# Kernel tuning notes

Hardware: AMD Instinct MI355X
Metric: run time of the kernel (lower is better)

## Reference

```python
import jax, jax.numpy as jnp
import numpy as np

GROUP_SIZE = 64  # int4 precision
QMAX = 7.0       # symmetric int4 quant scale divisor


def setup_inputs() -> dict:
    key = jax.random.key(0)
    ks = jax.random.split(key, 8)
    B, S, C_in, C_out, R = 1, 4096, 3072, 3072, 32
    G = C_in // GROUP_SIZE
    x = jax.random.normal(ks[0], (B, S, C_in), dtype=jnp.float32)
    # unpacked int4 weight codes in [0,16); reference subtracts 8 -> signed int4 [-8,7]
    qweight = jax.random.randint(ks[1], (C_out, C_in), 0, 16, dtype=jnp.int32)
    # small positive per-group, per-out-channel weight scales
    wscales = jax.random.uniform(ks[2], (G, C_out), dtype=jnp.float32) * 0.01 + 0.001
    # positive smoothing factors bounded away from zero
    smooth_factor = jax.random.uniform(ks[3], (C_in,), dtype=jnp.float32) + 0.5
    proj_down = jax.random.normal(ks[4], (C_in, R), dtype=jnp.float32) * (1.0 / np.sqrt(C_in))
    proj_up = jax.random.normal(ks[5], (C_out, R), dtype=jnp.float32) * (1.0 / np.sqrt(R))
    bias = jax.random.normal(ks[6], (C_out,), dtype=jnp.float32) * 0.02
    return {
        "x": x,
        "qweight": qweight,
        "wscales": wscales,
        "smooth_factor": smooth_factor,
        "proj_down": proj_down,
        "proj_up": proj_up,
        "bias": bias,
    }


def reference(x, qweight, wscales, smooth_factor, proj_down, proj_up, bias):
    B, S, C = x.shape
    C_out = qweight.shape[0]
    M = B * S
    G = C // GROUP_SIZE

    # --- smoothing: x_hat = x / s (SVDQuant smoothing on activations) ---
    xs = x.reshape(M, C) / smooth_factor  # (M, C)

    # --- low-rank branch hidden state (fused with quantization in CUDA kernel) ---
    lora_act = jnp.einsum('mc,cr->mr', xs, proj_down)  # (M, R)

    # --- dynamic per-token, per-group int4 activation quantization ---
    xg = xs.reshape(M, G, GROUP_SIZE)
    amax = jnp.max(jnp.abs(xg), axis=-1, keepdims=True)          # (M, G, 1)
    ascale = amax / QMAX
    q = jnp.clip(jnp.round(xg / jnp.maximum(ascale, 1e-8)), -8.0, 7.0)
    x_dq = (q * ascale).reshape(M, C)                            # dequantized activations

    # --- weight dequantization: signed int4 codes * per-group/out-channel scales ---
    qw = qweight.astype(jnp.float32) - 8.0                       # (C_out, C) in [-8, 7]
    w_dq = (qw.reshape(C_out, G, GROUP_SIZE) * wscales.T[:, :, None]).reshape(C_out, C)

    # --- quantized GEMM + low-rank correction + bias ---
    out = jnp.einsum('mc,oc->mo', x_dq, w_dq)
    out = out + jnp.einsum('mr,or->mo', lora_act, proj_up) + bias
    return out.reshape(B, S, C_out)
```

## Files before the change

kernel.cpp:

```cpp
#include <hip/hip_runtime.h>
#include <stdint.h>

typedef unsigned short u16;

#define MTOK 4096
#define CIN  3072
#define COUT 3072
#define RANK 32
#define KT48 48
#define RS   3136
#define LKSPLIT 16
#define LKC (CIN/LKSPLIT)


typedef __attribute__((ext_vector_type(8))) short bf16x8;
typedef __attribute__((ext_vector_type(4))) float f32x4;

__device__ __forceinline__ u16 f2bf(float f) {
  union { float f; unsigned u; } v; v.f = f;
  unsigned r = v.u + 0x7FFFu + ((v.u >> 16) & 1u);
  return (u16)(r >> 16);
}

__device__ __forceinline__ void gload_lds16(const void* g, void* l) {
  __builtin_amdgcn_global_load_lds(
      (const __attribute__((address_space(1))) unsigned int*)g,
      (__attribute__((address_space(3))) unsigned int*)l, 16, 0, 0);
}

__device__ __forceinline__ float quant1(float xs, float ascale, float qd) {
  float q = rintf(xs / qd);
  q = fminf(fmaxf(q, -8.f), 7.f);
  return q * ascale;
}


__global__ __launch_bounds__(256) void wdq_kernel(
    const int* __restrict__ qw, const float* __restrict__ wsc,
    const float* __restrict__ pu, u16* __restrict__ wdq, u16* __restrict__ pu_bf)
{
  const int o = blockIdx.x;
  const int t = threadIdx.x;
  const int4* qrow = (const int4*)(qw + (size_t)o * CIN);
  u16* orow = wdq + (size_t)o * RS;
#pragma unroll
  for (int p = 0; p < 3; ++p) {
    const int c4 = p * 256 + t;
    const int g = (c4 * 4) >> 6;
    const float ws = wsc[g * COUT + o];
    const int4 qv = qrow[c4];
    ushort4 ov;
    ov.x = f2bf((float)(qv.x - 8) * ws);
    ov.y = f2bf((float)(qv.y - 8) * ws);
    ov.z = f2bf((float)(qv.z - 8) * ws);
    ov.w = f2bf((float)(qv.w - 8) * ws);
    ((ushort4*)orow)[c4] = ov;
  }
  if (t < RANK) pu_bf[(size_t)o * RANK + t] = f2bf(pu[(size_t)o * RANK + t]);
}

__global__ __launch_bounds__(256) void quant_kernel(
    const float* __restrict__ x, const float* __restrict__ smooth,
    u16* __restrict__ xdq)
{
  const int b = blockIdx.x;
  const int t = threadIdx.x;
  const int m0 = (b >> 4) * 64;
  const int kblk = b & 15;
  const int col = (t & 15) * 4;
#pragma unroll
  for (int kt = 0; kt < 3; ++kt) {
    const int k0 = kblk * LKC + kt * 64;
#pragma unroll
    for (int it = 0; it < 4; ++it) {
      const int row = m0 + it * 16 + (t >> 4);
      const float4 xv = *(const float4*)(x + (size_t)row * CIN + k0 + col);
      const float4 sv = *(const float4*)(smooth + k0 + col);
      const float xs0 = xv.x / sv.x, xs1 = xv.y / sv.y;
      const float xs2 = xv.z / sv.z, xs3 = xv.w / sv.w;
      float a = fmaxf(fmaxf(fabsf(xs0), fabsf(xs1)), fmaxf(fabsf(xs2), fabsf(xs3)));
#pragma unroll
      for (int off = 1; off < 16; off <<= 1) a = fmaxf(a, __shfl_xor(a, off));
      const float ascale = a / 7.0f;
      const float qd = fmaxf(ascale, 1e-8f);
      ushort4 oq;
      oq.x = f2bf(quant1(xs0, ascale, qd));
      oq.y = f2bf(quant1(xs1, ascale, qd));
      oq.z = f2bf(quant1(xs2, ascale, qd));
      oq.w = f2bf(quant1(xs3, ascale, qd));
      *(ushort4*)(xdq + (size_t)row * RS + k0 + col) = oq;
    }
  }
}

__global__ __launch_bounds__(256) void lora_kernel(
    const float* __restrict__ x, const float* __restrict__ smooth,
    const float* __restrict__ pd, float* __restrict__ lp)
{
  __shared__ __align__(16) u16 sA[128 * 64];
  __shared__ __align__(16) u16 sB[32 * 64];
  const int b = blockIdx.x;
  const int t = threadIdx.x;
  const int m0 = (b >> 4) * 128;
  const int kblk = b & 15;
  const int wave = t >> 6, lane = t & 63;
  const int lm = lane & 15, lkq = (lane >> 4) * 8;

  f32x4 acc[2][2];
  const f32x4 fz = {0.f, 0.f, 0.f, 0.f};
#pragma unroll
  for (int i = 0; i < 2; ++i)
#pragma unroll
    for (int j = 0; j < 2; ++j) acc[i][j] = fz;

  for (int kt = 0; kt < LKC / 64; ++kt) {
    const int k0 = kblk * LKC + kt * 64;
    const int col = (t & 15) * 4;
#pragma unroll
    for (int it = 0; it < 8; ++it) {
      const int row = it * 16 + (t >> 4);
      const float4 xv = *(const float4*)(x + (size_t)(m0 + row) * CIN + k0 + col);
      const float4 sv = *(const float4*)(smooth + k0 + col);
      ushort4 ov;
      ov.x = f2bf(xv.x / sv.x); ov.y = f2bf(xv.y / sv.y);
      ov.z = f2bf(xv.z / sv.z); ov.w = f2bf(xv.w / sv.w);
      *(ushort4*)&sA[row * 64 + col] = ov;
    }
#pragma unroll
    for (int i = 0; i < 8; ++i) {
      const int idx = i * 256 + t;
      const int k = idx >> 5, r = idx & 31;
      sB[r * 64 + k] = f2bf(pd[(size_t)(k0 + k) * RANK + r]);
    }
    __syncthreads();
#pragma unroll
    for (int kk = 0; kk < 2; ++kk) {
      const int ko = kk * 32 + lkq;
      bf16x8 af[2], bfr[2];
#pragma unroll
      for (int i = 0; i < 2; ++i)
        af[i] = *(const bf16x8*)&sA[(wave * 32 + i * 16 + lm) * 64 + ko];
#pragma unroll
      for (int j = 0; j < 2; ++j)
        bfr[j] = *(const bf16x8*)&sB[(j * 16 + lm) * 64 + ko];
#pragma unroll
      for (int i = 0; i < 2; ++i)
#pragma unroll
        for (int j = 0; j < 2; ++j)
          acc[i][j] = __builtin_amdgcn_mfma_f32_16x16x32_bf16(af[i], bfr[j], acc[i][j], 0, 0, 0);
    }
    __syncthreads();
  }
  float* lpk = lp + (size_t)kblk * MTOK * RANK;
#pragma unroll
  for (int i = 0; i < 2; ++i)
#pragma unroll
    for (int j = 0; j < 2; ++j) {
      const int col = j * 16 + lm;
      const int row0 = m0 + wave * 32 + i * 16 + (lane >> 4) * 4;
#pragma unroll
      for (int r = 0; r < 4; ++r)
        lpk[(size_t)(row0 + r) * RANK + col] = acc[i][j][r];
    }
}

__global__ __launch_bounds__(256) void lora_fix_kernel(
    const float* __restrict__ lp, u16* __restrict__ lora_bf)
{
  const int idx = blockIdx.x * 256 + threadIdx.x;
  const int m = idx >> 5, c = idx & 31;
  float s = 0.f;
#pragma unroll
  for (int k = 0; k < LKSPLIT; ++k) s += lp[((size_t)k * MTOK + m) * RANK + c];
  lora_bf[(size_t)m * RANK + c] = f2bf(s);
}


__device__ __forceinline__ void stage_half(const u16* __restrict__ g, u16* lds_base,
                                           int kt, int half, int buf, int t) {
#pragma unroll
  for (int r = 0; r < 2; ++r) {
    const int ld = r * 512 + t;
    const int row = ld >> 3;
    const int d = ld & 7;
    const int c16 = d ^ (row & 7);
    gload_lds16(g + (size_t)(half * 128 + row) * RS + kt * 64 + c16 * 8,
                lds_base + buf * 16384 + half * 8192 + ld * 8);
  }
}

#define DSA(buf, mh) \
  _Pragma("unroll") for (int i = 0; i < 4; ++i) { \
    const int rl = wm * 64 + i * 16 + lm; \
    _Pragma("unroll") for (int kk = 0; kk < 2; ++kk) \
      af[i][kk] = *(const bf16x8*)&lds[(buf)*16384 + (mh)*8192 + rl * 64 + \
                    ((((kk << 2) | q4) ^ (rl & 7)) << 3)]; \
  }

#define DSB(buf, nh, BF) \
  _Pragma("unroll") for (int j = 0; j < 2; ++j) { \
    const int rl = wn * 32 + j * 16 + lm; \
    _Pragma("unroll") for (int kk = 0; kk < 2; ++kk) \
      BF[j][kk] = *(const bf16x8*)&lds[32768 + (buf)*16384 + (nh)*8192 + rl * 64 + \
                    ((((kk << 2) | q4) ^ (rl & 7)) << 3)]; \
  }

#define MFMA_Q(mh, nh, BF) \
  __builtin_amdgcn_s_setprio(1); \
  _Pragma("unroll") for (int i = 0; i < 4; ++i) \
  _Pragma("unroll") for (int j = 0; j < 2; ++j) \
  _Pragma("unroll") for (int kk = 0; kk < 2; ++kk) \
    acc[(mh)*4 + i][(nh)*2 + j] = __builtin_amdgcn_mfma_f32_16x16x32_bf16( \
        af[i][kk], BF[j][kk], acc[(mh)*4 + i][(nh)*2 + j], 0, 0, 0); \
  __builtin_amdgcn_s_setprio(0);

#define PH_OPEN() \
  __builtin_amdgcn_sched_barrier(0); \
  __builtin_amdgcn_s_barrier(); \
  asm volatile("s_waitcnt lgkmcnt(0)" ::: "memory"); \
  __builtin_amdgcn_sched_barrier(0)

#define PH_CLOSE() \
  __builtin_amdgcn_sched_barrier(0); \
  __builtin_amdgcn_s_barrier(); \
  __builtin_amdgcn_sched_barrier(0)

#define VM8() asm volatile("s_waitcnt vmcnt(8)" ::: "memory")
#define VM0() asm volatile("s_waitcnt vmcnt(0)" ::: "memory")

#define TILE8(cur, S_A0, S_B0, S_B1, S_A1, VMI) do { \
  DSA(cur, 0); DSB(cur, 0, bf0); \
  PH_OPEN(); MFMA_Q(0, 0, bf0); PH_CLOSE(); \
  DSB(cur, 1, bf1); S_A0; S_B0; \
  PH_OPEN(); MFMA_Q(0, 1, bf1); PH_CLOSE(); \
  DSA(cur, 1); S_B1; \
  PH_OPEN(); MFMA_Q(1, 1, bf1); PH_CLOSE(); \
  S_A1; \
  PH_OPEN(); MFMA_Q(1, 0, bf0); VMI; PH_CLOSE(); \
} while (0)

__global__ __launch_bounds__(512, 2) void gemm_kernel(
    const u16* __restrict__ xdq, const u16* __restrict__ wdq,
    const u16* __restrict__ pu_bf, const u16* __restrict__ lora_bf,
    const float* __restrict__ bias, float* __restrict__ out)
{
  __shared__ __align__(16) u16 lds[65536];

  const int t = threadIdx.x;
  const int wid = t >> 6, lane = t & 63;
  const int wm = wid >> 2, wn = wid & 3;
  const int lm = lane & 15, q4 = lane >> 4;

  const int wg = blockIdx.x;
  const int swz = (wg & 7) * 24 + (wg >> 3);
  const int by = swz / 12, bx = swz % 12;
  const int m0 = by * 256, n0 = bx * 256;

  const u16* Ag = xdq + (size_t)m0 * RS;
  const u16* Bg = wdq + (size_t)n0 * RS;
  u16* ldsB = lds + 32768;

  f32x4 acc[8][4];
  const f32x4 fz = {0.f, 0.f, 0.f, 0.f};
#pragma unroll
  for (int i = 0; i < 8; ++i)
#pragma unroll
    for (int j = 0; j < 4; ++j) acc[i][j] = fz;

  bf16x8 af[4][2], bf0[2][2], bf1[2][2];

  stage_half(Ag, lds,  0, 0, 0, t);
  stage_half(Bg, ldsB, 0, 0, 0, t);
  stage_half(Bg, ldsB, 0, 1, 0, t);
  stage_half(Ag, lds,  0, 1, 0, t);
  stage_half(Ag, lds,  1, 0, 1, t);
  stage_half(Bg, ldsB, 1, 0, 1, t);
  stage_half(Bg, ldsB, 1, 1, 1, t);
  stage_half(Ag, lds,  1, 1, 1, t);
  VM8();
  __builtin_amdgcn_s_barrier();
  __builtin_amdgcn_sched_barrier(0);

  for (int T = 0; T < 46; T += 2) {
    TILE8(0,
          stage_half(Ag, lds,  T + 2, 0, 0, t),
          stage_half(Bg, ldsB, T + 2, 0, 0, t),
          stage_half(Bg, ldsB, T + 2, 1, 0, t),
          stage_half(Ag, lds,  T + 2, 1, 0, t),
          VM8());
    TILE8(1,
          stage_half(Ag, lds,  T + 3, 0, 1, t),
          stage_half(Bg, ldsB, T + 3, 0, 1, t),
          stage_half(Bg, ldsB, T + 3, 1, 1, t),
          stage_half(Ag, lds,  T + 3, 1, 1, t),
          VM8());
  }
  TILE8(0, (void)0, (void)0, (void)0, (void)0, VM0());
  TILE8(1, (void)0, (void)0, (void)0, (void)0, (void)0);

  bf16x8 bl[4];
#pragma unroll
  for (int b = 0; b < 4; ++b) {
    const int bcol = n0 + (b >> 1) * 128 + wn * 32 + (b & 1) * 16 + lm;
    bl[b] = *(const bf16x8*)(pu_bf + (size_t)bcol * RANK + q4 * 8);
  }
#pragma unroll
  for (int a = 0; a < 8; ++a) {
    const int arow = m0 + (a >> 2) * 128 + wm * 64 + (a & 3) * 16 + lm;
    const bf16x8 al = *(const bf16x8*)(lora_bf + (size_t)arow * RANK + q4 * 8);
#pragma unroll
    for (int b = 0; b < 4; ++b)
      acc[a][b] = __builtin_amdgcn_mfma_f32_16x16x32_bf16(al, bl[b], acc[a][b], 0, 0, 0);
  }

#pragma unroll
  for (int b = 0; b < 4; ++b) {
    const int col = n0 + (b >> 1) * 128 + wn * 32 + (b & 1) * 16 + lm;
    const float bv = bias[col];
#pragma unroll
    for (int a = 0; a < 8; ++a) {
      const int row0 = m0 + (a >> 2) * 128 + wm * 64 + (a & 3) * 16 + q4 * 4;
#pragma unroll
      for (int r = 0; r < 4; ++r)
        out[(size_t)(row0 + r) * COUT + col] = acc[a][b][r] + bv;
    }
  }
}

extern "C" void kernel_launch(void* const* d_in, const int* in_sizes, int n_in,
                              void* d_out, int out_size, void* d_ws, size_t ws_size,
                              hipStream_t stream) {
  const float* x      = (const float*)d_in[0];
  const int*   qw     = (const int*)d_in[1];
  const float* wsc    = (const float*)d_in[2];
  const float* smooth = (const float*)d_in[3];
  const float* pd     = (const float*)d_in[4];
  const float* pu     = (const float*)d_in[5];
  const float* bias   = (const float*)d_in[6];
  float* out = (float*)d_out;

  u16* xdq     = (u16*)d_ws;
  u16* wdq     = xdq + (size_t)MTOK * RS;
  u16* pu_bf   = wdq + (size_t)COUT * RS;
  u16* lora_bf = pu_bf + (size_t)COUT * RANK;
  float* lp    = (float*)(lora_bf + (size_t)MTOK * RANK);

  wdq_kernel<<<COUT, 256, 0, stream>>>(qw, wsc, pu, wdq, pu_bf);
  quant_kernel<<<1024, 256, 0, stream>>>(x, smooth, xdq);
  lora_kernel<<<512, 256, 0, stream>>>(x, smooth, pd, lp);
  lora_fix_kernel<<<MTOK * RANK / 256, 256, 0, stream>>>(lp, lora_bf);
  gemm_kernel<<<192, 512, 0, stream>>>(
      xdq, wdq, pu_bf, lora_bf, bias, out);
}
```

Baseline: 251.8 us.

## Fuse weight dequant, activation quant and LoRA down-projection into one prep kernel

```diff
diff --git a/kernel.cpp b/kernel.cpp
--- a/kernel.cpp
+++ b/kernel.cpp
@@ -7,11 +7,10 @@
 #define CIN  3072
 #define COUT 3072
 #define RANK 32
-#define KT48 48
 #define RS   3136
 #define LKSPLIT 16
 #define LKC (CIN/LKSPLIT)
-
+#define WROWS 6
 
 typedef __attribute__((ext_vector_type(8))) short bf16x8;
 typedef __attribute__((ext_vector_type(4))) float f32x4;
@@ -34,50 +33,67 @@
   return q * ascale;
 }
 
-
-__global__ __launch_bounds__(256) void wdq_kernel(
+__global__ __launch_bounds__(256) void prep_kernel(
+    const float* __restrict__ x, const float* __restrict__ smooth,
     const int* __restrict__ qw, const float* __restrict__ wsc,
-    const float* __restrict__ pu, u16* __restrict__ wdq, u16* __restrict__ pu_bf)
-{
-  const int o = blockIdx.x;
-  const int t = threadIdx.x;
-  const int4* qrow = (const int4*)(qw + (size_t)o * CIN);
-  u16* orow = wdq + (size_t)o * RS;
-#pragma unroll
-  for (int p = 0; p < 3; ++p) {
-    const int c4 = p * 256 + t;
-    const int g = (c4 * 4) >> 6;
-    const float ws = wsc[g * COUT + o];
-    const int4 qv = qrow[c4];
-    ushort4 ov;
-    ov.x = f2bf((float)(qv.x - 8) * ws);
-    ov.y = f2bf((float)(qv.y - 8) * ws);
-    ov.z = f2bf((float)(qv.z - 8) * ws);
-    ov.w = f2bf((float)(qv.w - 8) * ws);
-    ((ushort4*)orow)[c4] = ov;
-  }
-  if (t < RANK) pu_bf[(size_t)o * RANK + t] = f2bf(pu[(size_t)o * RANK + t]);
-}
-
-__global__ __launch_bounds__(256) void quant_kernel(
-    const float* __restrict__ x, const float* __restrict__ smooth,
-    u16* __restrict__ xdq)
+    const float* __restrict__ pd, const float* __restrict__ pu,
+    u16* __restrict__ xdq, u16* __restrict__ wdq, u16* __restrict__ pu_bf,
+    float* __restrict__ lp)
 {
   const int b = blockIdx.x;
   const int t = threadIdx.x;
-  const int m0 = (b >> 4) * 64;
+
+#pragma unroll
+  for (int r = 0; r < WROWS; ++r) {
+    const int o = b * WROWS + r;
+    const int4* qrow = (const int4*)(qw + (size_t)o * CIN);
+    u16* orow = wdq + (size_t)o * RS;
+#pragma unroll
+    for (int p = 0; p < 3; ++p) {
+      const int c4 = p * 256 + t;
+      const int g = (c4 * 4) >> 6;
+      const float ws = wsc[g * COUT + o];
+      const int4 qv = qrow[c4];
+      ushort4 ov;
+      ov.x = f2bf((float)(qv.x - 8) * ws);
+      ov.y = f2bf((float)(qv.y - 8) * ws);
+      ov.z = f2bf((float)(qv.z - 8) * ws);
+      ov.w = f2bf((float)(qv.w - 8) * ws);
+      ((ushort4*)orow)[c4] = ov;
+    }
+  }
+  if (t < WROWS * RANK) {
+    const int o = b * WROWS + (t >> 5);
+    pu_bf[(size_t)o * RANK + (t & 31)] = f2bf(pu[(size_t)o * RANK + (t & 31)]);
+  }
+
+  __shared__ __align__(16) u16 sA[128 * 64];
+  __shared__ __align__(16) u16 sB[32 * 64];
+  const int m0 = (b >> 4) * 128;
   const int kblk = b & 15;
-  const int col = (t & 15) * 4;
-#pragma unroll
-  for (int kt = 0; kt < 3; ++kt) {
+  const int wave = t >> 6, lane = t & 63;
+  const int lm = lane & 15, lkq = (lane >> 4) * 8;
+
+  f32x4 acc[2][2];
+  const f32x4 fz = {0.f, 0.f, 0.f, 0.f};
+#pragma unroll
+  for (int i = 0; i < 2; ++i)
+#pragma unroll
+    for (int j = 0; j < 2; ++j) acc[i][j] = fz;
+
+  for (int kt = 0; kt < LKC / 64; ++kt) {
     const int k0 = kblk * LKC + kt * 64;
-#pragma unroll
-    for (int it = 0; it < 4; ++it) {
-      const int row = m0 + it * 16 + (t >> 4);
-      const float4 xv = *(const float4*)(x + (size_t)row * CIN + k0 + col);
+    const int col = (t & 15) * 4;
+#pragma unroll
+    for (int it = 0; it < 8; ++it) {
+      const int row = it * 16 + (t >> 4);
+      const float4 xv = *(const float4*)(x + (size_t)(m0 + row) * CIN + k0 + col);
       const float4 sv = *(const float4*)(smooth + k0 + col);
       const float xs0 = xv.x / sv.x, xs1 = xv.y / sv.y;
       const float xs2 = xv.z / sv.z, xs3 = xv.w / sv.w;
+      ushort4 ov;
+      ov.x = f2bf(xs0); ov.y = f2bf(xs1); ov.z = f2bf(xs2); ov.w = f2bf(xs3);
+      *(ushort4*)&sA[row * 64 + col] = ov;
       float a = fmaxf(fmaxf(fabsf(xs0), fabsf(xs1)), fmaxf(fabsf(xs2), fabsf(xs3)));
 #pragma unroll
       for (int off = 1; off < 16; off <<= 1) a = fmaxf(a, __shfl_xor(a, off));
@@ -88,43 +104,7 @@
       oq.y = f2bf(quant1(xs1, ascale, qd));
       oq.z = f2bf(quant1(xs2, ascale, qd));
       oq.w = f2bf(quant1(xs3, ascale, qd));
-      *(ushort4*)(xdq + (size_t)row * RS + k0 + col) = oq;
-    }
-  }
-}
-
-__global__ __launch_bounds__(256) void lora_kernel(
-    const float* __restrict__ x, const float* __restrict__ smooth,
-    const float* __restrict__ pd, float* __restrict__ lp)
-{
-  __shared__ __align__(16) u16 sA[128 * 64];
-  __shared__ __align__(16) u16 sB[32 * 64];
-  const int b = blockIdx.x;
-  const int t = threadIdx.x;
-  const int m0 = (b >> 4) * 128;
-  const int kblk = b & 15;
-  const int wave = t >> 6, lane = t & 63;
-  const int lm = lane & 15, lkq = (lane >> 4) * 8;
-
-  f32x4 acc[2][2];
-  const f32x4 fz = {0.f, 0.f, 0.f, 0.f};
-#pragma unroll
-  for (int i = 0; i < 2; ++i)
-#pragma unroll
-    for (int j = 0; j < 2; ++j) acc[i][j] = fz;
-
-  for (int kt = 0; kt < LKC / 64; ++kt) {
-    const int k0 = kblk * LKC + kt * 64;
-    const int col = (t & 15) * 4;
-#pragma unroll
-    for (int it = 0; it < 8; ++it) {
-      const int row = it * 16 + (t >> 4);
-      const float4 xv = *(const float4*)(x + (size_t)(m0 + row) * CIN + k0 + col);
-      const float4 sv = *(const float4*)(smooth + k0 + col);
-      ushort4 ov;
-      ov.x = f2bf(xv.x / sv.x); ov.y = f2bf(xv.y / sv.y);
-      ov.z = f2bf(xv.z / sv.z); ov.w = f2bf(xv.w / sv.w);
-      *(ushort4*)&sA[row * 64 + col] = ov;
+      *(ushort4*)(xdq + (size_t)(m0 + row) * RS + k0 + col) = oq;
     }
 #pragma unroll
     for (int i = 0; i < 8; ++i) {
@@ -345,9 +325,8 @@
   u16* lora_bf = pu_bf + (size_t)COUT * RANK;
   float* lp    = (float*)(lora_bf + (size_t)MTOK * RANK);
 
-  wdq_kernel<<<COUT, 256, 0, stream>>>(qw, wsc, pu, wdq, pu_bf);
-  quant_kernel<<<1024, 256, 0, stream>>>(x, smooth, xdq);
-  lora_kernel<<<512, 256, 0, stream>>>(x, smooth, pd, lp);
+  prep_kernel<<<512, 256, 0, stream>>>(
+      x, smooth, qw, wsc, pd, pu, xdq, wdq, pu_bf, lp);
   lora_fix_kernel<<<MTOK * RANK / 256, 256, 0, stream>>>(lp, lora_bf);
   gemm_kernel<<<192, 512, 0, stream>>>(
       xdq, wdq, pu_bf, lora_bf, bias, out);
```

Measured after the change: 229.7 us. 8.8% less time.
